# Kernel tuning notes

Hardware: AMD Instinct MI355X
Metric: run time of the kernel (lower is better)

Reference implementation:

```python
import jax, jax.numpy as jnp
import numpy as np

TEMPERATURE = 10.0
CE_WEIGHT = 10.0
NUM_CLUSTERS = 32  # clusters per batch element, labels in [0, K)


def setup_inputs() -> dict:
    key = jax.random.key(0)
    k1, k2, k3, k4, k5 = jax.random.split(key, 5)
    B, N, D, C, K = 4, 2048, 2, 64, NUM_CLUSTERS
    embedding = jax.random.normal(k1, (B, N, D), dtype=jnp.float32)
    contr_emb = jax.random.normal(k2, (B, N, C), dtype=jnp.float32)
    abs_coords = jax.random.normal(k3, (B, N, D), dtype=jnp.float32)
    patch_mask = jax.random.randint(k4, (B, N, N), 0, 2, dtype=jnp.int32)
    cluster_labels = jax.random.randint(k5, (B, N), 0, K, dtype=jnp.int32)
    return {
        "embedding": embedding,
        "contr_emb": contr_emb,
        "abs_coords": abs_coords,
        "patch_mask": patch_mask,
        "cluster_labels": cluster_labels,
    }


def reference(embedding, contr_emb, abs_coords, patch_mask, cluster_labels):
    B, N, D = embedding.shape
    C = contr_emb.shape[-1]
    K = NUM_CLUSTERS

    # --- anchor term: pairwise distance + nonlinearity + masked mean ---
    # diff[b,i,j,:] = (e_i - e_j) + (c_i - c_j)
    diff = (embedding[:, :, None] - embedding[:, None]) + (
        abs_coords[:, :, None] - abs_coords[:, None]
    )  # [B,N,N,D]
    dist_sq = jnp.sum(diff * diff, axis=-1)  # norm(2)^2, [B,N,N]
    nonlinear_dist = 1.0 - jnp.exp(-dist_sq / TEMPERATURE)
    m = (patch_mask == 1).astype(nonlinear_dist.dtype)
    loss = jnp.sum(nonlinear_dist * m) / jnp.sum(m)  # masked mean

    # --- contrastive term ---
    # F.normalize(contr_emb, dim=-1)
    norm = jnp.maximum(jnp.linalg.norm(contr_emb, axis=-1, keepdims=True), 1e-12)
    c = contr_emb / norm  # [B,N,C]

    # per-batch cluster means under no_grad (stop_gradient)
    onehot = jax.nn.one_hot(cluster_labels, K, dtype=c.dtype)  # [B,N,K]
    sums = jnp.einsum("bnc,bnk->bkc", c, onehot)  # [B,K,C]
    counts = jnp.maximum(jnp.sum(onehot, axis=1), 1.0)  # [B,K]
    means = jax.lax.stop_gradient(sums / counts[..., None])  # [B,K,C]

    # cat per-batch [C,K] matrices along cluster axis -> [C, B*K]
    cum_mean_clusters = means.reshape(B * K, C).T
    stacked = c.reshape(B * N, C)
    logits = stacked @ cum_mean_clusters  # [B*N, B*K]

    target = cluster_labels.reshape(-1)  # labels as written (no batch offset)
    logp = jax.nn.log_softmax(logits, axis=-1)
    nll = -jnp.take_along_axis(logp, target[:, None].astype(jnp.int32), axis=1)[:, 0]
    bce_loss = jnp.mean(nll)  # all targets >= 0, so no ignore_index hits

    return loss + CE_WEIGHT * bce_loss
```

## Files before the change

### kernel.cpp

```cpp
#include <hip/hip_runtime.h>
#include <math.h>

#define B_ 4
#define N_ 2048
#define C_ 64
#define K_ 32
#define BN_ (B_ * N_)

#define WS_NLL 0
#define WS_INVN 64
#define WS_SX 8320
#define WS_SY 16512
#define WS_MEANS 24704
#define WS_APART 32896

typedef const __attribute__((address_space(1))) void* gas_ptr;
typedef __attribute__((address_space(3))) void* las_ptr;

__global__ __launch_bounds__(256) void k_prep(
    const float* __restrict__ emb, const float* __restrict__ absc,
    const float* __restrict__ contr, float* __restrict__ ws) {
  int t = threadIdx.x, lane = t & 63, w = t >> 6;
  int flat = blockIdx.x * 256 + t;
  if (flat == 0) ws[WS_NLL] = 0.0f;
  if (flat < BN_) {
    float2 ev = ((const float2*)emb)[flat];
    float2 av = ((const float2*)absc)[flat];
    ws[WS_SX + flat] = ev.x + av.x;
    ws[WS_SY + flat] = ev.y + av.y;
  }
  int row = blockIdx.x * 4 + w;
  float x = contr[row * C_ + lane];
  float ss = x * x;
#pragma unroll
  for (int off = 32; off > 0; off >>= 1) ss += __shfl_xor(ss, off);
  if (lane == 0) ws[WS_INVN + row] = 1.0f / fmaxf(sqrtf(ss), 1e-12f);
}

__global__ __launch_bounds__(256) void k_cluster(
    const float* __restrict__ contr, const int* __restrict__ labels,
    float* __restrict__ ws) {
  __shared__ int lsLab[N_];
  __shared__ float lsum[4][64];
  __shared__ float lcnt[4];
  int t = threadIdx.x, lane = t & 63, w = t >> 6;
  int b = blockIdx.x >> 5, k = blockIdx.x & 31;
  const int4* lab4 = (const int4*)(labels + b * N_);
  int4* l4 = (int4*)lsLab;
  l4[t] = lab4[t];
  l4[t + 256] = lab4[t + 256];
  __syncthreads();
  float acc = 0.0f, cnt = 0.0f;
  for (int g0 = w * 512; g0 < w * 512 + 512; g0 += 64) {
    unsigned long long mb = __ballot(lsLab[g0 + lane] == k);
    while (mb) {
      int bit = __ffsll((unsigned long long)mb) - 1;
      mb &= mb - 1;
      int r = b * N_ + g0 + bit;
      float inv = ws[WS_INVN + r];
      acc += contr[(size_t)r * C_ + lane] * inv;
      cnt += 1.0f;
    }
  }
  lsum[w][lane] = acc;
  if (lane == 0) lcnt[w] = cnt;
  __syncthreads();
  if (t < 64) {
    float s = lsum[0][t] + lsum[1][t] + lsum[2][t] + lsum[3][t];
    float c = lcnt[0] + lcnt[1] + lcnt[2] + lcnt[3];
    ws[WS_MEANS + (b * K_ + k) * C_ + t] = s / fmaxf(c, 1.0f);
  }
}

__global__ __launch_bounds__(128) void k_logits_nll(
    const float* __restrict__ contr, const int* __restrict__ labels,
    float* __restrict__ ws) {
  __shared__ float lc[32 * C_];
  __shared__ float lm[2][32], lsv[2][32], ltl[32];
  int t = threadIdx.x, lane = t & 63, w = t >> 6;
  int r0 = blockIdx.x * 32;
  int j = w * 64 + lane;
  const float4* mean4 = (const float4*)(ws + WS_MEANS);
  float4 mk[16];
#pragma unroll
  for (int q = 0; q < 16; ++q) mk[q] = mean4[j * 16 + q];
  const float4* c4 = (const float4*)(contr + (size_t)r0 * C_);
  float4* lc4 = (float4*)lc;
  lc4[t] = c4[t];
  lc4[t + 128] = c4[t + 128];
  lc4[t + 256] = c4[t + 256];
  lc4[t + 384] = c4[t + 384];
  __syncthreads();
  for (int r = 0; r < 32; ++r) {
    const float4* cr = lc4 + r * 16;
    float acc = 0.0f;
#pragma unroll
    for (int q = 0; q < 16; ++q) {
      float4 cv = cr[q];
      acc += cv.x * mk[q].x + cv.y * mk[q].y + cv.z * mk[q].z + cv.w * mk[q].w;
    }
    acc *= ws[WS_INVN + r0 + r];
    float m = acc;
#pragma unroll
    for (int off = 32; off > 0; off >>= 1) m = fmaxf(m, __shfl_xor(m, off));
    float s = __expf(acc - m);
#pragma unroll
    for (int off = 32; off > 0; off >>= 1) s += __shfl_xor(s, off);
    int tgt = labels[r0 + r];
    float tl = __shfl(acc, tgt);
    if (lane == 0) {
      lm[w][r] = m;
      lsv[w][r] = s;
      if (w == 0) ltl[r] = tl;
    }
  }
  __syncthreads();
  if (t < 32) {
    float m0 = lm[0][t], m1 = lm[1][t];
    float mm = fmaxf(m0, m1);
    float ss = lsv[0][t] * __expf(m0 - mm) + lsv[1][t] * __expf(m1 - mm);
    float nll = (mm + __logf(ss)) - ltl[t];
#pragma unroll
    for (int off = 16; off > 0; off >>= 1) nll += __shfl_xor(nll, off);
    if (t == 0) atomicAdd(&ws[WS_NLL], nll);
  }
}

__device__ __forceinline__ void pair4(float sx, float sy, float4 xs, float4 ys,
                                      int4 m, float& acc, int& cnt) {
  float dx, dy, d2, v;
  dx = sx - xs.x; dy = sy - ys.x; d2 = dx * dx + dy * dy;
  v = 1.0f - __expf(d2 * -0.1f);
  if (m.x == 1) { acc += v; cnt += 1; }
  dx = sx - xs.y; dy = sy - ys.y; d2 = dx * dx + dy * dy;
  v = 1.0f - __expf(d2 * -0.1f);
  if (m.y == 1) { acc += v; cnt += 1; }
  dx = sx - xs.z; dy = sy - ys.z; d2 = dx * dx + dy * dy;
  v = 1.0f - __expf(d2 * -0.1f);
  if (m.z == 1) { acc += v; cnt += 1; }
  dx = sx - xs.w; dy = sy - ys.w; d2 = dx * dx + dy * dy;
  v = 1.0f - __expf(d2 * -0.1f);
  if (m.w == 1) { acc += v; cnt += 1; }
}

__global__ __launch_bounds__(256) void k_anchor(
    const int* __restrict__ mask, float* __restrict__ ws) {
  __shared__ int4 stage[2048];
  __shared__ float red[8];
  int t = threadIdx.x, lane = t & 63, w = t >> 6;
  int g = blockIdx.x;
  int b = g >> 9;
  int rbase = (g & 511) * 4;
  const float* sxp = ws + WS_SX + b * N_;
  const float* syp = ws + WS_SY + b * N_;
  const char* gbase = (const char*)(mask + (size_t)(b * N_ + rbase) * N_);
#pragma unroll
  for (int i = 0; i < 8; ++i) {
    int ci = i * 256 + w * 64;
    __builtin_amdgcn_global_load_lds(
        (gas_ptr)(gbase + (size_t)(ci + lane) * 16),
        (las_ptr)&stage[ci], 16, 0, 0);
  }
  float4 xsA = *(const float4*)(sxp + t * 4);
  float4 ysA = *(const float4*)(syp + t * 4);
  float4 xsB = *(const float4*)(sxp + 1024 + t * 4);
  float4 ysB = *(const float4*)(syp + 1024 + t * 4);
  float rx[4], ry[4];
#pragma unroll
  for (int r = 0; r < 4; ++r) { rx[r] = sxp[rbase + r]; ry[r] = syp[rbase + r]; }
  asm volatile("s_waitcnt vmcnt(0)" ::: "memory");
  float acc = 0.0f;
  int cnt = 0;
#pragma unroll
  for (int i = 0; i < 8; ++i) {
    int4 m = stage[i * 256 + t];
    pair4(rx[i >> 1], ry[i >> 1], (i & 1) ? xsB : xsA, (i & 1) ? ysB : ysA,
          m, acc, cnt);
  }
  float cntf = (float)cnt;
#pragma unroll
  for (int off = 32; off > 0; off >>= 1) {
    acc += __shfl_xor(acc, off);
    cntf += __shfl_xor(cntf, off);
  }
  if (lane == 0) { red[w * 2] = acc; red[w * 2 + 1] = cntf; }
  __syncthreads();
  if (t == 0) {
    ws[WS_APART + g * 2 + 0] = red[0] + red[2] + red[4] + red[6];
    ws[WS_APART + g * 2 + 1] = red[1] + red[3] + red[5] + red[7];
  }
}

__global__ __launch_bounds__(256) void k_final(
    const float* __restrict__ ws, float* __restrict__ out) {
  __shared__ float red[8];
  int t = threadIdx.x, lane = t & 63, w = t >> 6;
  float a = 0.0f, c = 0.0f;
  for (int i = t; i < 2048; i += 256) {
    a += ws[WS_APART + i * 2 + 0];
    c += ws[WS_APART + i * 2 + 1];
  }
#pragma unroll
  for (int off = 32; off > 0; off >>= 1) {
    a += __shfl_xor(a, off);
    c += __shfl_xor(c, off);
  }
  if (lane == 0) { red[w * 2] = a; red[w * 2 + 1] = c; }
  __syncthreads();
  if (t == 0) {
    float at = red[0] + red[2] + red[4] + red[6];
    float ct = red[1] + red[3] + red[5] + red[7];
    out[0] = at / ct + 10.0f * ws[WS_NLL] * (1.0f / (float)BN_);
  }
}

extern "C" void kernel_launch(void* const* d_in, const int* in_sizes, int n_in,
                              void* d_out, int out_size, void* d_ws, size_t ws_size,
                              hipStream_t stream) {
  const float* emb    = (const float*)d_in[0];
  const float* contr  = (const float*)d_in[1];
  const float* absc   = (const float*)d_in[2];
  const int*   mask   = (const int*)d_in[3];
  const int*   labels = (const int*)d_in[4];
  float* ws  = (float*)d_ws;
  float* out = (float*)d_out;

  k_prep<<<2048, 256, 0, stream>>>(emb, absc, contr, ws);
  k_cluster<<<B_ * K_, 256, 0, stream>>>(contr, labels, ws);
  k_logits_nll<<<256, 128, 0, stream>>>(contr, labels, ws);
  k_anchor<<<2048, 256, 0, stream>>>(mask, ws);
  k_final<<<1, 256, 0, stream>>>(ws, out);
}
```

Baseline: 146.3 us.

## Stream mask directly into registers with grid-strided anchor blocks, halving grid

The anchor kernel no longer stages the mask through LDS with global_load_lds. Each thread now issues direct int4 global loads at a large stride across the whole mask, doing 16 chunks per thread, and the grid is halved to 1024 blocks. The aim is to cut LDS staging and the per-block wait, and to keep more independent loads in flight per thread. The cost is per-chunk row coordinate loads from global memory and a different coalescing pattern, and the final reduction loop is adjusted to match the new block count.

Result: no change. 146.9 us (+0.4%).

```diff
diff --git a/kernel.cpp b/kernel.cpp
--- a/kernel.cpp
+++ b/kernel.cpp
@@ -13,9 +13,6 @@
 #define WS_SY 16512
 #define WS_MEANS 24704
 #define WS_APART 32896
-
-typedef const __attribute__((address_space(1))) void* gas_ptr;
-typedef __attribute__((address_space(3))) void* las_ptr;
 
 __global__ __launch_bounds__(256) void k_prep(
     const float* __restrict__ emb, const float* __restrict__ absc,
@@ -145,37 +142,29 @@
 
 __global__ __launch_bounds__(256) void k_anchor(
     const int* __restrict__ mask, float* __restrict__ ws) {
-  __shared__ int4 stage[2048];
   __shared__ float red[8];
   int t = threadIdx.x, lane = t & 63, w = t >> 6;
-  int g = blockIdx.x;
-  int b = g >> 9;
-  int rbase = (g & 511) * 4;
-  const float* sxp = ws + WS_SX + b * N_;
-  const float* syp = ws + WS_SY + b * N_;
-  const char* gbase = (const char*)(mask + (size_t)(b * N_ + rbase) * N_);
-#pragma unroll
-  for (int i = 0; i < 8; ++i) {
-    int ci = i * 256 + w * 64;
-    __builtin_amdgcn_global_load_lds(
-        (gas_ptr)(gbase + (size_t)(ci + lane) * 16),
-        (las_ptr)&stage[ci], 16, 0, 0);
-  }
-  float4 xsA = *(const float4*)(sxp + t * 4);
-  float4 ysA = *(const float4*)(syp + t * 4);
-  float4 xsB = *(const float4*)(sxp + 1024 + t * 4);
-  float4 ysB = *(const float4*)(syp + 1024 + t * 4);
-  float rx[4], ry[4];
-#pragma unroll
-  for (int r = 0; r < 4; ++r) { rx[r] = sxp[rbase + r]; ry[r] = syp[rbase + r]; }
-  asm volatile("s_waitcnt vmcnt(0)" ::: "memory");
+  int flat = blockIdx.x * 256 + t;
+  int cg = flat & 511;
+  const int4* m4 = (const int4*)mask;
+  const float* wsx = ws + WS_SX;
+  const float* wsy = ws + WS_SY;
+  const float4* sx4 = (const float4*)wsx;
+  const float4* sy4 = (const float4*)wsy;
   float acc = 0.0f;
   int cnt = 0;
 #pragma unroll
-  for (int i = 0; i < 8; ++i) {
-    int4 m = stage[i * 256 + t];
-    pair4(rx[i >> 1], ry[i >> 1], (i & 1) ? xsB : xsA, (i & 1) ? ysB : ysA,
-          m, acc, cnt);
+  for (int bt = 0; bt < 4; ++bt) {
+    float4 xs = sx4[bt * 512 + cg];
+    float4 ys = sy4[bt * 512 + cg];
+#pragma unroll
+    for (int j = 0; j < 4; ++j) {
+      int idx = flat + (bt * 4 + j) * 262144;
+      int4 m = m4[idx];
+      int row = idx >> 9;
+      float rx = wsx[row], ry = wsy[row];
+      pair4(rx, ry, xs, ys, m, acc, cnt);
+    }
   }
   float cntf = (float)cnt;
 #pragma unroll
@@ -186,8 +175,8 @@
   if (lane == 0) { red[w * 2] = acc; red[w * 2 + 1] = cntf; }
   __syncthreads();
   if (t == 0) {
-    ws[WS_APART + g * 2 + 0] = red[0] + red[2] + red[4] + red[6];
-    ws[WS_APART + g * 2 + 1] = red[1] + red[3] + red[5] + red[7];
+    ws[WS_APART + blockIdx.x * 2 + 0] = red[0] + red[2] + red[4] + red[6];
+    ws[WS_APART + blockIdx.x * 2 + 1] = red[1] + red[3] + red[5] + red[7];
   }
 }
 
@@ -196,7 +185,7 @@
   __shared__ float red[8];
   int t = threadIdx.x, lane = t & 63, w = t >> 6;
   float a = 0.0f, c = 0.0f;
-  for (int i = t; i < 2048; i += 256) {
+  for (int i = t; i < 1024; i += 256) {
     a += ws[WS_APART + i * 2 + 0];
     c += ws[WS_APART + i * 2 + 1];
   }
@@ -228,6 +217,6 @@
   k_prep<<<2048, 256, 0, stream>>>(emb, absc, contr, ws);
   k_cluster<<<B_ * K_, 256, 0, stream>>>(contr, labels, ws);
   k_logits_nll<<<256, 128, 0, stream>>>(contr, labels, ws);
-  k_anchor<<<2048, 256, 0, stream>>>(mask, ws);
+  k_anchor<<<1024, 256, 0, stream>>>(mask, ws);
   k_final<<<1, 256, 0, stream>>>(ws, out);
 }
```
